# Kernel optimization log

Measured on AMD Instinct MI355X. Metric: run time of the kernel, lower is better.

The kernel has to match this reference:

```python
import jax, jax.numpy as jnp
import numpy as np

N, D, E, NNZ = 200000, 128, 1024, 1600000


def setup_inputs() -> dict:
    key = jax.random.key(0)
    ks = jax.random.split(key, 8)
    x = jax.random.normal(ks[0], (N, D), jnp.float32)
    tb_W = jax.random.normal(ks[1], (5, 3, D, D), jnp.float32) * 0.05
    tb_b = jax.random.normal(ks[2], (5, 3, D), jnp.float32) * 0.05
    hg_W = jax.random.normal(ks[3], (2, D, D), jnp.float32) * 0.05
    hg_b = jax.random.normal(ks[4], (2, D), jnp.float32) * 0.05
    hyperedge_attr = jax.random.normal(ks[5], (E, D), jnp.float32)
    node_idx = jax.random.randint(ks[6], (NNZ,), 0, N)
    edge_idx = jax.random.randint(ks[7], (NNZ,), 0, E)
    return dict(x=x, tb_W=tb_W, tb_b=tb_b, hg_W=hg_W, hg_b=hg_b,
                hyperedge_attr=hyperedge_attr, node_idx=node_idx,
                edge_idx=edge_idx, num_hyperedges=E)


def _time_block(x, W, b):
    # 1x1 Conv2d over channel dim == per-node linear. W:[3,D,D], b:[3,D]
    c1 = x @ W[0] + b[0]
    c2 = x @ W[1] + b[1]
    c3 = x @ W[2] + b[2]
    return jax.nn.relu(c1 + jax.nn.sigmoid(c2) + c3)


def _hypergraph_conv(x, node_idx, edge_idx, W, b, num_nodes, num_edges):
    # PyG HypergraphConv, use_attention=False (heads=1):
    # out = D^{-1} H B H^T (x W) + b, H given as COO (node_idx, edge_idx)
    xp = x @ W
    ones = jnp.ones(node_idx.shape[0], xp.dtype)
    Dn = jax.ops.segment_sum(ones, node_idx, num_segments=num_nodes)
    Dn = jnp.where(Dn > 0, 1.0 / Dn, 0.0)
    Be = jax.ops.segment_sum(ones, edge_idx, num_segments=num_edges)
    Be = jnp.where(Be > 0, 1.0 / Be, 0.0)
    # node -> hyperedge aggregation, normalized by 1/B_e
    m = jax.ops.segment_sum(xp[node_idx], edge_idx, num_segments=num_edges) * Be[:, None]
    # hyperedge -> node aggregation, normalized by 1/D_v
    out = jax.ops.segment_sum(m[edge_idx], node_idx, num_segments=num_nodes) * Dn[:, None]
    return out + b


def reference(x, tb_W, tb_b, hg_W, hg_b, hyperedge_attr, node_idx, edge_idx, num_hyperedges):
    # hyperedge_attr is unused when use_attention=False (faithful to PyG)
    n = x.shape[0]
    h = _time_block(x, tb_W[0], tb_b[0])
    h = _hypergraph_conv(h, node_idx, edge_idx, hg_W[0], hg_b[0], n, num_hyperedges)
    h = _time_block(h, tb_W[1], tb_b[1])
    h = _time_block(h, tb_W[2], tb_b[2])
    h = _hypergraph_conv(h, node_idx, edge_idx, hg_W[1], hg_b[1], n, num_hyperedges)
    h = _time_block(h, tb_W[3], tb_b[3])
    h = _time_block(h, tb_W[4], tb_b[4])
    return h
```

## Files before the change

### kernel.cpp

```cpp
#include <hip/hip_runtime.h>
#include <stdint.h>

#define N_NODES 200000
#define DIM     128
#define N_EDGES 1024
#define NNZ_C   1600000
#define NT64    3125

#define NBLK   250
#define CHUNK  6400
#define ITERS  25
#define NCB    196

#define NG_BLOCKS 2000
#define NG_WAVES  (NG_BLOCKS*4)
#define NG_K      25
#define NG_STAGE  512

typedef __attribute__((ext_vector_type(8))) short short8;
typedef __attribute__((ext_vector_type(4))) float f32x4;

__device__ __forceinline__ float u2f(uint32_t u){ union{uint32_t u;float f;} x; x.u=u; return x.f; }
__device__ __forceinline__ uint32_t f2u(float f){ union{uint32_t u;float f;} x; x.f=f; return x.u; }
__device__ __forceinline__ unsigned short f2bf(float f){
  uint32_t u = f2u(f);
  u += 0x7fffu + ((u >> 16) & 1u);
  return (unsigned short)(u >> 16);
}
__device__ __forceinline__ float fsig(float x){
  float e = __builtin_amdgcn_exp2f(x * -1.44269504088896340736f);
  return __builtin_amdgcn_rcpf(1.f + e);
}

__global__ void prep_tb_w(const float* __restrict__ W, short* __restrict__ Wt){
  int i = blockIdx.x*256 + threadIdx.x;
  if (i >= 5*256*128) return;
  int k   = i & 127;
  int col = (i >> 7) & 255;
  int s   = i >> 15;
  int j = col >> 7, n = col & 127;
  float v;
  if (j == 0)
    v = W[((s*3 + 0)*128 + k)*128 + n] + W[((s*3 + 2)*128 + k)*128 + n];
  else
    v = W[((s*3 + 1)*128 + k)*128 + n];
  Wt[i] = (short)f2bf(v);
}
__global__ void prep_hg_wf(const float* __restrict__ W, float* __restrict__ Wtf){
  int i = blockIdx.x*256 + threadIdx.x;
  if (i >= 2*128*128) return;
  int k = i & 127;
  int n = (i >> 7) & 127;
  int g = i >> 14;
  Wtf[i] = W[(g*128 + k)*128 + n];
}

__global__ __launch_bounds__(256) void hist_kernel(
    const int* __restrict__ nidx, const int* __restrict__ eidx,
    int* __restrict__ ebh, int* __restrict__ nbh)
{
  __shared__ int eh[N_EDGES];
  __shared__ int nh[NCB];
  int tid = threadIdx.x, blk = blockIdx.x;
  #pragma unroll
  for (int l = tid; l < N_EDGES; l += 256) eh[l] = 0;
  for (int l = tid; l < NCB; l += 256) nh[l] = 0;
  __syncthreads();
  int base = blk*CHUNK;
  for (int it = 0; it < ITERS; it++){
    int i = base + it*256 + tid;
    atomicAdd(&eh[eidx[i]], 1);
    atomicAdd(&nh[nidx[i] >> 10], 1);
  }
  __syncthreads();
  for (int l = tid; l < N_EDGES; l += 256) ebh[blk*N_EDGES + l] = eh[l];
  for (int l = tid; l < NCB; l += 256) nbh[blk*NCB + l] = nh[l];
}

__global__ __launch_bounds__(1024) void scan_kernel(
    int* __restrict__ ebh, int* __restrict__ eoff,
    int* __restrict__ nbh, int* __restrict__ cbase)
{
  __shared__ int sc[1024];
  int tid = threadIdx.x;
  if (blockIdx.x == 0){
    int e = tid;
    int total = 0;
    #pragma unroll 10
    for (int b = 0; b < NBLK; b++){
      int idx = b*N_EDGES + e;
      int t = ebh[idx];
      ebh[idx] = total;
      total += t;
    }
    sc[e] = total; __syncthreads();
    for (int off=1; off<1024; off<<=1){
      int v = (e >= off) ? sc[e-off] : 0;
      __syncthreads();
      sc[e] += v;
      __syncthreads();
    }
    int base = sc[e] - total;
    eoff[e] = base;
    if (e == 1023) eoff[1024] = sc[1023];
    #pragma unroll 10
    for (int b = 0; b < NBLK; b++) ebh[b*N_EDGES + e] += base;
  } else {
    int c = tid;
    int total = 0;
    if (c < NCB){
      #pragma unroll 10
      for (int b = 0; b < NBLK; b++){
        int idx = b*NCB + c;
        int t = nbh[idx];
        nbh[idx] = total;
        total += t;
      }
    }
    if (c < 256) sc[c] = (c < NCB) ? total : 0;
    __syncthreads();
    for (int off=1; off<256; off<<=1){
      int v = (c < 256 && c >= off) ? sc[c-off] : 0;
      __syncthreads();
      if (c < 256) sc[c] += v;
      __syncthreads();
    }
    if (c < NCB){
      int base = sc[c] - total;
      cbase[c] = base;
      if (c == NCB-1) cbase[NCB] = sc[c];
      #pragma unroll 10
      for (int b = 0; b < NBLK; b++) nbh[b*NCB + c] += base;
    }
  }
}

__global__ __launch_bounds__(256) void scatter_kernel(
    const int* __restrict__ nidx, const int* __restrict__ eidx,
    const int* __restrict__ ebh, const int* __restrict__ nbh,
    int* __restrict__ enodes, uint32_t* __restrict__ pairs)
{
  __shared__ int cure[N_EDGES];
  __shared__ int curn[NCB];
  int tid = threadIdx.x, blk = blockIdx.x;
  for (int l = tid; l < N_EDGES; l += 256) cure[l] = ebh[blk*N_EDGES + l];
  for (int l = tid; l < NCB; l += 256)     curn[l] = nbh[blk*NCB + l];
  __syncthreads();
  int base = blk*CHUNK;
  for (int it = 0; it < ITERS; it++){
    int i = base + it*256 + tid;
    int v = nidx[i], e = eidx[i];
    int pe = atomicAdd(&cure[e], 1);
    enodes[pe] = v;
    int pn = atomicAdd(&curn[v >> 10], 1);
    pairs[pn] = ((uint32_t)v << 10) | (uint32_t)e;
  }
}

__global__ __launch_bounds__(256) void node_build_kernel(
    const uint32_t* __restrict__ pairs, const int* __restrict__ cbase,
    int* __restrict__ noff, int* __restrict__ nedges)
{
  __shared__ int cnt[1024];
  __shared__ int off[1024];
  __shared__ int part[256];
  int tid = threadIdx.x, c = blockIdx.x;
  int n0 = c << 10;
  int nloc = min(1024, N_NODES - n0);
  int s = cbase[c], e = cbase[c+1];
  #pragma unroll
  for (int l = tid; l < 1024; l += 256) cnt[l] = 0;
  __syncthreads();
  for (int i = s + tid; i < e; i += 256)
    atomicAdd(&cnt[(pairs[i] >> 10) & 1023], 1);
  __syncthreads();
  int c0 = cnt[tid*4], c1 = cnt[tid*4+1], c2 = cnt[tid*4+2], c3 = cnt[tid*4+3];
  int sum = c0+c1+c2+c3;
  part[tid] = sum; __syncthreads();
  for (int o=1; o<256; o<<=1){
    int v = (tid >= o) ? part[tid-o] : 0;
    __syncthreads();
    part[tid] += v;
    __syncthreads();
  }
  int pb = part[tid] - sum;
  off[tid*4]   = pb;
  off[tid*4+1] = pb + c0;
  off[tid*4+2] = pb + c0 + c1;
  off[tid*4+3] = pb + c0 + c1 + c2;
  __syncthreads();
  for (int l = tid; l < nloc; l += 256) noff[n0 + l] = s + off[l];
  if (c == 0 && tid == 0) noff[N_NODES] = NNZ_C;
  __syncthreads();
  for (int i = s + tid; i < e; i += 256){
    uint32_t p = pairs[i];
    int local = (p >> 10) & 1023;
    int pos = s + atomicAdd(&off[local], 1);
    nedges[pos] = (int)((p & 1023) << 8);
  }
}

template<bool IN_F32, int OUT_MODE>
__global__ __launch_bounds__(512, 6) void gemm_kernel(
    const void* __restrict__ in, void* __restrict__ out,
    const short* __restrict__ Wt, const float* __restrict__ bias)
{
  __shared__ short Atile[64][136];
  const int tid  = threadIdx.x;
  const int lane = tid & 63;
  const int w    = tid >> 6;
  const int l15  = lane & 15;
  const int quad = lane >> 4;
  const int ncol = w*16 + l15;

  short8 bfrag[2][4];
  #pragma unroll
  for (int j = 0; j < 2; j++){
    const short* bp = Wt + (j*128 + ncol)*128 + quad*8;
    #pragma unroll
    for (int ks = 0; ks < 4; ks++)
      bfrag[j][ks] = *(const short8*)(bp + ks*32);
  }
  float bv13 = bias[ncol] + bias[256 + ncol];
  float bv2  = bias[128 + ncol];

  const int arow = tid >> 4;
  const int aseg = tid & 15;

  short8 pre0, pre1;
  auto loadA = [&](int t){
    int off0 = (t*64 + arow)*128 + aseg*8;
    int off1 = off0 + 32*128;
    if (IN_F32){
      const float* f = (const float*)in;
      #pragma unroll
      for (int h = 0; h < 2; h++){
        const float* fp = f + (h ? off1 : off0);
        f32x4 q0 = *(const f32x4*)fp;
        f32x4 q1 = *(const f32x4*)(fp + 4);
        short8 t0;
        #pragma unroll
        for (int u = 0; u < 4; u++){
          t0[u]   = (short)f2bf(q0[u]);
          t0[u+4] = (short)f2bf(q1[u]);
        }
        if (h) pre1 = t0; else pre0 = t0;
      }
    } else {
      pre0 = *(const short8*)((const short*)in + off0);
      pre1 = *(const short8*)((const short*)in + off1);
    }
  };

  int t = blockIdx.x;
  loadA(t);
  for (;;){
    __syncthreads();
    *(short8*)&Atile[arow][aseg*8]      = pre0;
    *(short8*)&Atile[arow + 32][aseg*8] = pre1;
    __syncthreads();
    int tn = t + gridDim.x;
    if (tn < NT64) loadA(tn);

    const int base = t*64;
    #pragma unroll
    for (int rt = 0; rt < 4; rt++){
      short8 af[4];
      #pragma unroll
      for (int ks = 0; ks < 4; ks++)
        af[ks] = *(const short8*)&Atile[rt*16 + l15][ks*32 + quad*8];

      f32x4 acc[2];
      #pragma unroll
      for (int j = 0; j < 2; j++){
        acc[j] = (f32x4){0.f, 0.f, 0.f, 0.f};
        #pragma unroll
        for (int ks = 0; ks < 4; ks++)
          acc[j] = __builtin_amdgcn_mfma_f32_16x16x32_bf16(
              af[ks], bfrag[j][ks], acc[j], 0, 0, 0);
      }

      #pragma unroll
      for (int r = 0; r < 4; r++){
        int row = base + rt*16 + quad*4 + r;
        float sg = fsig(acc[1][r] + bv2);
        float v = acc[0][r] + bv13 + sg;
        v = fmaxf(v, 0.f);
        if (OUT_MODE == 1) ((float*)out)[row*128 + ncol] = v;
        else if (OUT_MODE == 0) ((unsigned short*)out)[row*128 + ncol] = f2bf(v);
        else {
          int pk = __builtin_amdgcn_cvt_pk_fp8_f32(v, v, 0, false);
          ((unsigned char*)out)[row*128 + ncol] = (unsigned char)(pk & 0xff);
        }
      }
    }
    if (tn >= NT64) break;
    t = tn;
  }
}

__device__ __forceinline__ void acc16(float* a, uint4 r){
  uint32_t w[4] = {r.x, r.y, r.z, r.w};
  #pragma unroll
  for (int q = 0; q < 4; q++){
    auto lo = __builtin_amdgcn_cvt_pk_f32_fp8(w[q], false);
    auto hi = __builtin_amdgcn_cvt_pk_f32_fp8(w[q], true);
    a[q*4+0] += lo[0]; a[q*4+1] += lo[1]; a[q*4+2] += hi[0]; a[q*4+3] += hi[1];
  }
}

__global__ __launch_bounds__(256) void edge_gather_kernel(
    const unsigned char* __restrict__ h8, const int* __restrict__ eoff,
    const int* __restrict__ enodes, const float* __restrict__ Wtf,
    uint32_t* __restrict__ mbf)
{
  int e = blockIdx.x;
  int s = eoff[e], en = eoff[e+1];
  int tid  = threadIdx.x;
  int slot = tid >> 3;
  int ch   = tid & 7;
  const size_t choff = (size_t)ch * 16;

  float a[16];
  #pragma unroll
  for (int j = 0; j < 16; j++) a[j] = 0.f;

  int i0 = s + slot;
  int n0 = (i0      < en) ? enodes[i0]      : -1;
  int n1 = (i0 + 32 < en) ? enodes[i0 + 32] : -1;
  int n2 = (i0 + 64 < en) ? enodes[i0 + 64] : -1;
  int n3 = (i0 + 96 < en) ? enodes[i0 + 96] : -1;

  while (i0 < en){
    int i1 = i0 + 128;
    int m0 = (i1      < en) ? enodes[i1]      : -1;
    int m1 = (i1 + 32 < en) ? enodes[i1 + 32] : -1;
    int m2 = (i1 + 64 < en) ? enodes[i1 + 64] : -1;
    int m3 = (i1 + 96 < en) ? enodes[i1 + 96] : -1;

    uint4 r0 = *(const uint4*)(h8 + (((size_t)max(n0,0)) << 7) + choff);
    uint4 r1 = *(const uint4*)(h8 + (((size_t)max(n1,0)) << 7) + choff);
    uint4 r2 = *(const uint4*)(h8 + (((size_t)max(n2,0)) << 7) + choff);
    uint4 r3 = *(const uint4*)(h8 + (((size_t)max(n3,0)) << 7) + choff);
    if (n0 < 0) r0 = make_uint4(0,0,0,0);
    if (n1 < 0) r1 = make_uint4(0,0,0,0);
    if (n2 < 0) r2 = make_uint4(0,0,0,0);
    if (n3 < 0) r3 = make_uint4(0,0,0,0);

    acc16(a, r0); acc16(a, r1); acc16(a, r2); acc16(a, r3);

    n0 = m0; n1 = m1; n2 = m2; n3 = m3;
    i0 = i1;
  }

  __shared__ float red[32][132];
  __shared__ float srow[128];
  __shared__ float sacc[128];
  #pragma unroll
  for (int j = 0; j < 16; j++) red[slot][ch*16 + j] = a[j];
  __syncthreads();
  if (tid < 128){
    float sum = 0.f;
    #pragma unroll
    for (int r = 0; r < 32; r++) sum += red[r][tid];
    srow[tid] = sum;
  }
  __syncthreads();
  int deg = en - s;
  float be = deg > 0 ? 1.f/(float)deg : 0.f;
  if (tid < 128){
    const f32x4* w4 = (const f32x4*)(Wtf + tid*128);
    float acc = 0.f;
    #pragma unroll
    for (int k = 0; k < 32; k++){
      f32x4 qv = w4[k];
      acc += qv[0]*srow[k*4] + qv[1]*srow[k*4+1] + qv[2]*srow[k*4+2] + qv[3]*srow[k*4+3];
    }
    sacc[tid] = acc * be;
  }
  __syncthreads();
  if (tid < 64){
    uint32_t lo = f2bf(sacc[2*tid]);
    uint32_t hi = f2bf(sacc[2*tid+1]);
    mbf[e*64 + tid] = (hi << 16) | lo;
  }
}

__global__ __launch_bounds__(256) void node_gather_kernel(
    const uint32_t* __restrict__ mbf, const int* __restrict__ noff,
    const int* __restrict__ nedges, const float* __restrict__ hb,
    uint32_t* __restrict__ outp)
{
  __shared__ int sidx[4][NG_STAGE];
  const int wslot = threadIdx.x >> 6;
  const int wid   = (blockIdx.x << 2) | wslot;
  const int lane  = threadIdx.x & 63;
  const int lane4 = lane << 2;
  const float b0 = hb[2*lane], b1 = hb[2*lane+1];
  const int v0 = wid * NG_K;

  int eArr = noff[min(v0 + 1 + lane, N_NODES)];
  int sW   = __builtin_amdgcn_readfirstlane(noff[v0]);
  int send = __builtin_amdgcn_readlane(eArr, NG_K - 1);
  int n = send - sW;

  int* myIdx = sidx[wslot];
  bool useLds = (n <= NG_STAGE);
  if (useLds){
    for (int b = lane; b < n; b += 64) myIdx[b] = nedges[sW + b];
  }
  __syncthreads();

  const char* mb = (const char*)mbf;
  if (useLds){
    int s = sW;
    for (int vr = 0; vr < NG_K; vr++){
      int e = __builtin_amdgcn_readlane(eArr, vr);
      float a0 = 0.f, a1 = 0.f;
      uint32_t rlast = 0;
      for (int i = s; i < e; i += 8){
        uint32_t r[8];
        #pragma unroll
        for (int k = 0; k < 8; k++){
          int li = min(i + k, e - 1) - sW;
          r[k] = *(const uint32_t*)(mb + (myIdx[li] + lane4));
        }
        #pragma unroll
        for (int k = 0; k < 8; k++){
          a0 += u2f(r[k] << 16);
          a1 += u2f(r[k] & 0xffff0000u);
        }
        rlast = r[7];
      }
      int d = e - s;
      float dead = (float)(((d + 7) & ~7) - d);
      a0 -= dead * u2f(rlast << 16);
      a1 -= dead * u2f(rlast & 0xffff0000u);
      float dn = (d > 0) ? 1.f/(float)d : 0.f;
      uint32_t lo = f2bf(a0*dn + b0);
      uint32_t hi = f2bf(a1*dn + b1);
      outp[((size_t)(v0 + vr) << 6) | lane] = (hi << 16) | lo;
      s = e;
    }
  } else {
    int s = sW;
    for (int vr = 0; vr < NG_K; vr++){
      int e = __builtin_amdgcn_readlane(eArr, vr);
      float a0 = 0.f, a1 = 0.f;
      for (int i = s; i < e; i++){
        uint32_t r = *(const uint32_t*)(mb + (nedges[i] + lane4));
        a0 += u2f(r << 16);
        a1 += u2f(r & 0xffff0000u);
      }
      int d = e - s;
      float dn = (d > 0) ? 1.f/(float)d : 0.f;
      uint32_t lo = f2bf(a0*dn + b0);
      uint32_t hi = f2bf(a1*dn + b1);
      outp[((size_t)(v0 + vr) << 6) | lane] = (hi << 16) | lo;
      s = e;
    }
  }
}

extern "C" void kernel_launch(void* const* d_in, const int* in_sizes, int n_in,
                              void* d_out, int out_size, void* d_ws, size_t ws_size,
                              hipStream_t stream)
{
  (void)in_sizes; (void)n_in; (void)out_size; (void)ws_size;
  const float* x   = (const float*)d_in[0];
  const float* tbW = (const float*)d_in[1];
  const float* tbb = (const float*)d_in[2];
  const float* hgW = (const float*)d_in[3];
  const float* hgb = (const float*)d_in[4];
  const int* nidx  = (const int*)d_in[6];
  const int* eidx  = (const int*)d_in[7];
  float* out = (float*)d_out;

  char* p = (char*)d_ws;
  auto alloc = [&](size_t sz){ void* r = (void*)p; p += (sz + 255) & ~(size_t)255; return r; };
  unsigned short* hA = (unsigned short*)alloc((size_t)N_NODES*DIM*2);
  unsigned short* hB = (unsigned short*)alloc((size_t)N_NODES*DIM*2);
  unsigned char*  h8 = (unsigned char*)alloc((size_t)N_NODES*DIM);
  uint32_t* mbf = (uint32_t*)alloc((size_t)N_EDGES*64*4);
  short* WtTb = (short*)alloc((size_t)5*256*128*2);
  float* Wtf  = (float*)alloc((size_t)2*128*128*4);
  int* ebh  = (int*)alloc((size_t)NBLK*N_EDGES*4);
  int* nbh  = (int*)alloc((size_t)NBLK*NCB*4);
  int* eoff = (int*)alloc((N_EDGES+1)*4);
  int* cbase= (int*)alloc((NCB+1)*4);
  int* noff = (int*)alloc((size_t)(N_NODES+1)*4);
  int* enodes = (int*)alloc((size_t)NNZ_C*4);
  int* nedges = (int*)alloc((size_t)NNZ_C*4 + 64);
  uint32_t* pairs = (uint32_t*)alloc((size_t)NNZ_C*4);

  static hipStream_t s2 = nullptr;
  static hipEvent_t evFork = nullptr, evCsr = nullptr;
  if (!s2){
    hipStreamCreateWithFlags(&s2, hipStreamNonBlocking);
    hipEventCreateWithFlags(&evFork, hipEventDisableTiming);
    hipEventCreateWithFlags(&evCsr, hipEventDisableTiming);
  }

  hipEventRecord(evFork, stream);
  hipStreamWaitEvent(s2, evFork, 0);
  hist_kernel<<<NBLK, 256, 0, s2>>>(nidx, eidx, ebh, nbh);
  scan_kernel<<<2, 1024, 0, s2>>>(ebh, eoff, nbh, cbase);
  scatter_kernel<<<NBLK, 256, 0, s2>>>(nidx, eidx, ebh, nbh, enodes, pairs);
  node_build_kernel<<<NCB, 256, 0, s2>>>(pairs, cbase, noff, nedges);
  hipEventRecord(evCsr, s2);

  prep_tb_w<<<640, 256, 0, stream>>>(tbW, WtTb);
  prep_hg_wf<<<128, 256, 0, stream>>>(hgW, Wtf);
  gemm_kernel<true, 2><<<1250, 512, 0, stream>>>(x, h8, WtTb, tbb);

  hipStreamWaitEvent(stream, evCsr, 0);
  edge_gather_kernel<<<N_EDGES, 256, 0, stream>>>(h8, eoff, enodes, Wtf, mbf);
  node_gather_kernel<<<NG_BLOCKS, 256, 0, stream>>>(mbf, noff, nedges, hgb, (uint32_t*)hA);
  gemm_kernel<false, 0><<<1250, 512, 0, stream>>>(hA, hB, WtTb + 1*32768, tbb + 1*384);
  gemm_kernel<false, 2><<<1250, 512, 0, stream>>>(hB, h8, WtTb + 2*32768, tbb + 2*384);
  edge_gather_kernel<<<N_EDGES, 256, 0, stream>>>(h8, eoff, enodes, Wtf + 16384, mbf);
  node_gather_kernel<<<NG_BLOCKS, 256, 0, stream>>>(mbf, noff, nedges, hgb + 128, (uint32_t*)hA);
  gemm_kernel<false, 0><<<1250, 512, 0, stream>>>(hA, hB, WtTb + 3*32768, tbb + 3*384);
  gemm_kernel<false, 1><<<1250, 512, 0, stream>>>(hB, out, WtTb + 4*32768, tbb + 4*384);
}
```

Before: 616.6 us.

## Double-buffer GEMM A tiles via direct global-to-LDS loads with XOR swizzle

For the bf16-input GEMM path, A tiles are now loaded with global_load_lds straight into a double-buffered LDS tile. The next tile is fetched while the current one is computed, so there is one barrier per iteration and no register staging. The padded LDS layout is replaced by an XOR swizzle of 16-byte groups, which the fp32-input path also uses, to avoid bank conflicts without padding. The code relies on the asynchronous LDS writes finishing before the barrier. It also doubles LDS use for the bf16 variant, which may affect occupancy.

```diff
diff --git a/kernel.cpp b/kernel.cpp
--- a/kernel.cpp
+++ b/kernel.cpp
@@ -205,13 +205,13 @@
     const void* __restrict__ in, void* __restrict__ out,
     const short* __restrict__ Wt, const float* __restrict__ bias)
 {
-  __shared__ short Atile[64][136];
+  __shared__ short Atile[IN_F32 ? 1 : 2][64][128];
   const int tid  = threadIdx.x;
   const int lane = tid & 63;
-  const int w    = tid >> 6;
+  const int wv   = tid >> 6;
   const int l15  = lane & 15;
   const int quad = lane >> 4;
-  const int ncol = w*16 + l15;
+  const int ncol = wv*16 + l15;
 
   short8 bfrag[2][4];
   #pragma unroll
@@ -224,14 +224,78 @@
   float bv13 = bias[ncol] + bias[256 + ncol];
   float bv2  = bias[128 + ncol];
 
-  const int arow = tid >> 4;
-  const int aseg = tid & 15;
-
-  short8 pre0, pre1;
-  auto loadA = [&](int t){
-    int off0 = (t*64 + arow)*128 + aseg*8;
-    int off1 = off0 + 32*128;
-    if (IN_F32){
+  auto computeTile = [&](int t, int b){
+    const int base = t*64;
+    #pragma unroll
+    for (int rt = 0; rt < 4; rt++){
+      const int rr = rt*16 + l15;
+      const int sw = rr & 7;
+      short8 af[4];
+      #pragma unroll
+      for (int ks = 0; ks < 4; ks++)
+        af[ks] = *(const short8*)&Atile[b][rr][((ks*4 + quad) ^ sw)*8];
+
+      f32x4 acc[2];
+      #pragma unroll
+      for (int j = 0; j < 2; j++){
+        acc[j] = (f32x4){0.f, 0.f, 0.f, 0.f};
+        #pragma unroll
+        for (int ks = 0; ks < 4; ks++)
+          acc[j] = __builtin_amdgcn_mfma_f32_16x16x32_bf16(
+              af[ks], bfrag[j][ks], acc[j], 0, 0, 0);
+      }
+
+      #pragma unroll
+      for (int r = 0; r < 4; r++){
+        int row = base + rt*16 + quad*4 + r;
+        float sg = fsig(acc[1][r] + bv2);
+        float v = acc[0][r] + bv13 + sg;
+        v = fmaxf(v, 0.f);
+        if (OUT_MODE == 1) ((float*)out)[row*128 + ncol] = v;
+        else if (OUT_MODE == 0) ((unsigned short*)out)[row*128 + ncol] = f2bf(v);
+        else {
+          int pk = __builtin_amdgcn_cvt_pk_fp8_f32(v, v, 0, false);
+          ((unsigned char*)out)[row*128 + ncol] = (unsigned char)(pk & 0xff);
+        }
+      }
+    }
+  };
+
+  if constexpr (!IN_F32){
+    const int lrow = lane >> 4;
+    const int lgr  = lane & 15;
+    auto dmaLoad = [&](int t, int b){
+      #pragma unroll
+      for (int h = 0; h < 2; h++){
+        int r = h*32 + wv*4 + lrow;
+        int g = lgr ^ (r & 7);
+        const short* gp = (const short*)in + ((size_t)(t*64 + r))*128 + g*8;
+        short* lp = &Atile[b][h*32 + wv*4][0];
+        __builtin_amdgcn_global_load_lds(
+            (const __attribute__((address_space(1))) void*)gp,
+            (__attribute__((address_space(3))) void*)lp,
+            16, 0, 0);
+      }
+    };
+
+    int t = blockIdx.x;
+    int p = 0;
+    dmaLoad(t, 0);
+    for (;;){
+      __syncthreads();
+      int tn = t + gridDim.x;
+      if (tn < NT64) dmaLoad(tn, p ^ 1);
+      computeTile(t, p);
+      if (tn >= NT64) break;
+      t = tn; p ^= 1;
+    }
+  } else {
+    const int arow = tid >> 4;
+    const int aseg = tid & 15;
+    short8 pre0, pre1;
+    auto loadA = [&](int t){
+      int off0 = (t*64 + arow)*128 + aseg*8;
+      int off1 = off0 + 32*128;
       const float* f = (const float*)in;
       #pragma unroll
       for (int h = 0; h < 2; h++){
@@ -246,56 +310,22 @@
         }
         if (h) pre1 = t0; else pre0 = t0;
       }
-    } else {
-      pre0 = *(const short8*)((const short*)in + off0);
-      pre1 = *(const short8*)((const short*)in + off1);
-    }
-  };
-
-  int t = blockIdx.x;
-  loadA(t);
-  for (;;){
-    __syncthreads();
-    *(short8*)&Atile[arow][aseg*8]      = pre0;
-    *(short8*)&Atile[arow + 32][aseg*8] = pre1;
-    __syncthreads();
-    int tn = t + gridDim.x;
-    if (tn < NT64) loadA(tn);
-
-    const int base = t*64;
-    #pragma unroll
-    for (int rt = 0; rt < 4; rt++){
-      short8 af[4];
-      #pragma unroll
-      for (int ks = 0; ks < 4; ks++)
-        af[ks] = *(const short8*)&Atile[rt*16 + l15][ks*32 + quad*8];
-
-      f32x4 acc[2];
-      #pragma unroll
-      for (int j = 0; j < 2; j++){
-        acc[j] = (f32x4){0.f, 0.f, 0.f, 0.f};
-        #pragma unroll
-        for (int ks = 0; ks < 4; ks++)
-          acc[j] = __builtin_amdgcn_mfma_f32_16x16x32_bf16(
-              af[ks], bfrag[j][ks], acc[j], 0, 0, 0);
-      }
-
-      #pragma unroll
-      for (int r = 0; r < 4; r++){
-        int row = base + rt*16 + quad*4 + r;
-        float sg = fsig(acc[1][r] + bv2);
-        float v = acc[0][r] + bv13 + sg;
-        v = fmaxf(v, 0.f);
-        if (OUT_MODE == 1) ((float*)out)[row*128 + ncol] = v;
-        else if (OUT_MODE == 0) ((unsigned short*)out)[row*128 + ncol] = f2bf(v);
-        else {
-          int pk = __builtin_amdgcn_cvt_pk_fp8_f32(v, v, 0, false);
-          ((unsigned char*)out)[row*128 + ncol] = (unsigned char)(pk & 0xff);
-        }
-      }
-    }
-    if (tn >= NT64) break;
-    t = tn;
+    };
+
+    int t = blockIdx.x;
+    loadA(t);
+    const int swz = arow & 7;
+    for (;;){
+      __syncthreads();
+      *(short8*)&Atile[0][arow][(aseg ^ swz)*8]      = pre0;
+      *(short8*)&Atile[0][arow + 32][(aseg ^ swz)*8] = pre1;
+      __syncthreads();
+      int tn = t + gridDim.x;
+      if (tn < NT64) loadA(tn);
+      computeTile(t, 0);
+      if (tn >= NT64) break;
+      t = tn;
+    }
   }
 }
 
```

Result: no change. 622.4 us (+0.9%).
